# Kernel optimization log

Measured on AMD Instinct MI355X. Metric: run time of the kernel, lower is better.

## Reference

```python
import jax, jax.numpy as jnp
import numpy as np
import math

IN_DIM = 1024
OUT_DIM = 1024
GRID_SIZE = 5
SPLINE_ORDER = 3
N_COEFFS = GRID_SIZE + SPLINE_ORDER          # 8
N_KNOTS = GRID_SIZE + 2 * SPLINE_ORDER + 1   # 12
EPS = 1e-08


def setup_inputs() -> dict:
    key = jax.random.key(0)
    k_x, k_c, k_w = jax.random.split(key, 3)
    B = 4096
    x = jax.random.normal(k_x, (B, IN_DIM), dtype=jnp.float32)
    coeffs = jax.random.normal(k_c, (OUT_DIM, IN_DIM * N_COEFFS), dtype=jnp.float32) * 0.1
    # kaiming_uniform(a=sqrt(5)) -> U(-bound, bound), bound = sqrt(6/((1+a^2)*fan_in)) = 1/sqrt(fan_in)
    bound = 1.0 / math.sqrt(IN_DIM)
    base_weight = jax.random.uniform(k_w, (OUT_DIM, IN_DIM), dtype=jnp.float32,
                                     minval=-bound, maxval=bound)
    step = 2.0 / GRID_SIZE
    init_val = math.log(math.exp(step) - 1.0)
    grid_steps_log = jnp.full((IN_DIM, N_KNOTS - 1), init_val, dtype=jnp.float32)
    grid_start = jnp.full((IN_DIM, 1), -1.0 - SPLINE_ORDER * step, dtype=jnp.float32)
    res_scale = jnp.zeros((1,), dtype=jnp.float32)
    return {"x": x, "coeffs": coeffs, "base_weight": base_weight,
            "grid_steps_log": grid_steps_log, "grid_start": grid_start,
            "res_scale": res_scale}


def _get_grid(grid_steps_log, grid_start):
    steps = jax.nn.softplus(grid_steps_log)            # [in, n_knots-1]
    grid = jnp.concatenate([grid_start, steps], axis=-1)
    return jnp.cumsum(grid, axis=-1)                   # [in, n_knots]


def _b_spline(x, grid):
    # x: [B, in], grid: [in, n_knots] -> bases: [B, in, n_coeffs]
    x_u = x[:, :, None]                                # [B, in, 1]
    g = grid[None, :, :]                               # [1, in, n_knots]
    bases = ((x_u >= g[:, :, :-1]) & (x_u < g[:, :, 1:])).astype(x.dtype)
    for d in range(1, SPLINE_ORDER + 1):
        left = (x_u - g[:, :, :-(d + 1)]) / (g[:, :, d:-1] - g[:, :, :-(d + 1)] + EPS)
        right = (g[:, :, d + 1:] - x_u) / (g[:, :, d + 1:] - g[:, :, 1:-d] + EPS)
        bases = left * bases[:, :, :-1] + right * bases[:, :, 1:]
    return bases


def reference(x, coeffs, base_weight, grid_steps_log, grid_start, res_scale):
    grid = _get_grid(grid_steps_log, grid_start)
    spline_basis = _b_spline(x, grid)                  # [B, in, n_coeffs]
    B = spline_basis.shape[0]
    spline_flat = spline_basis.reshape(B, -1)          # [B, in*n_coeffs]
    spline_out = spline_flat @ coeffs.T                # [B, out]
    base_out = jax.nn.silu(x) @ base_weight.T          # [B, out]
    y = spline_out + base_out
    y = y + res_scale * x                              # residual (in_dim == out_dim)
    return y
```

## Files before the change

kernel.cpp:

```cpp
#include <hip/hip_runtime.h>

#define IN_DIM   1024
#define OUT_DIM  1024
#define BATCH    4096
#define NC       8
#define NK       12
#define KSPLINE  (IN_DIM * NC)
#define KDIM     (KSPLINE + IN_DIM)
#define EPS      1e-8f

#define NBLK_A   ((IN_DIM / 256) * (BATCH / 16))
#define NBLK_W   ((OUT_DIM * (KDIM / 4)) / 256)

#define BM       128
#define BN       64
#define BKQ      32
#define NKT      (KDIM / BKQ)
#define NGBLK    ((BATCH / BM) * (OUT_DIM / BN))

#define SWZ(r)   (((r) >> 1) & 3)

typedef _Float16 f16x8  __attribute__((ext_vector_type(8)));
typedef float    f32x4  __attribute__((ext_vector_type(4)));

static __device__ __forceinline__ unsigned short f2h_bits(float f) {
  _Float16 h = (_Float16)f;
  return __builtin_bit_cast(unsigned short, h);
}

static __device__ __forceinline__ void gl_lds16(const unsigned short* g, unsigned short* l) {
  __builtin_amdgcn_global_load_lds(
      (const __attribute__((address_space(1))) unsigned int*)g,
      (__attribute__((address_space(3))) unsigned int*)l, 16, 0, 0);
}

__global__ __launch_bounds__(256) void prep_k(const float* __restrict__ x,
                                              const float* __restrict__ coeffs,
                                              const float* __restrict__ bw,
                                              const float* __restrict__ gsl,
                                              const float* __restrict__ gstart,
                                              const float* __restrict__ rsp,
                                              unsigned short* __restrict__ A,
                                              unsigned short* __restrict__ W,
                                              float* __restrict__ out) {
  const int blk = blockIdx.x;
  if (blk < NBLK_A) {
    const int i  = (blk & 3) * 256 + threadIdx.x;
    const int b0 = (blk >> 2) * 16;
    const float rs = rsp[0];
    float g[NK];
    float acc = gstart[i];
    g[0] = acc;
#pragma unroll
    for (int t = 0; t < NK - 1; ++t) {
      float v  = gsl[i * (NK - 1) + t];
      float sp = (v > 20.f) ? v : log1pf(expf(v));
      acc += sp;
      g[t + 1] = acc;
    }
    float r[30];
#pragma unroll
    for (int j = 0; j < 11; ++j) r[j]      = 1.f / (g[j + 1] - g[j] + EPS);
#pragma unroll
    for (int j = 0; j < 10; ++j) r[11 + j] = 1.f / (g[j + 2] - g[j] + EPS);
#pragma unroll
    for (int j = 0; j <  9; ++j) r[21 + j] = 1.f / (g[j + 3] - g[j] + EPS);

    for (int bb = 0; bb < 16; ++bb) {
      const int b = b0 + bb;
      float xv = x[(size_t)b * IN_DIM + i];
      float bas[NK - 1];
#pragma unroll
      for (int k = 0; k < NK - 1; ++k)
        bas[k] = (xv >= g[k] && xv < g[k + 1]) ? 1.f : 0.f;
      const int off[3] = {0, 11, 21};
#pragma unroll
      for (int d = 1; d <= 3; ++d) {
#pragma unroll
        for (int k = 0; k < NK - 1 - d; ++k) {
          float left  = (xv - g[k])         * r[off[d - 1] + k];
          float right = (g[k + d + 1] - xv) * r[off[d - 1] + k + 1];
          bas[k] = left * bas[k] + right * bas[k + 1];
        }
      }
      uint4 pack;
      pack.x = (unsigned)f2h_bits(bas[0]) | ((unsigned)f2h_bits(bas[1]) << 16);
      pack.y = (unsigned)f2h_bits(bas[2]) | ((unsigned)f2h_bits(bas[3]) << 16);
      pack.z = (unsigned)f2h_bits(bas[4]) | ((unsigned)f2h_bits(bas[5]) << 16);
      pack.w = (unsigned)f2h_bits(bas[6]) | ((unsigned)f2h_bits(bas[7]) << 16);
      *(uint4*)&A[(size_t)b * KDIM + i * NC] = pack;
      float s = xv / (1.f + expf(-xv));
      A[(size_t)b * KDIM + KSPLINE + i] = f2h_bits(s);
      out[(size_t)b * OUT_DIM + i] = rs * xv;
    }
  } else {
    int idx = (blk - NBLK_A) * 256 + threadIdx.x;
    int n  = idx / (KDIM / 4);
    int k4 = (idx - n * (KDIM / 4)) * 4;
    float4 v;
    if (k4 < KSPLINE) v = *(const float4*)&coeffs[(size_t)n * KSPLINE + k4];
    else              v = *(const float4*)&bw[(size_t)n * IN_DIM + (k4 - KSPLINE)];
    ushort4 o;
    o.x = f2h_bits(v.x); o.y = f2h_bits(v.y); o.z = f2h_bits(v.z); o.w = f2h_bits(v.w);
    *(ushort4*)&W[(size_t)n * KDIM + k4] = o;
  }
}

__global__ __launch_bounds__(256, 2) void gemm_k(const unsigned short* __restrict__ A,
                                                 const unsigned short* __restrict__ W,
                                                 float* __restrict__ out) {
  __shared__ __align__(16) unsigned short As[4][BM][BKQ];
  __shared__ __align__(16) unsigned short Bs[4][BN][BKQ];
  const int tid  = threadIdx.x;
  const int wave = tid >> 6;
  const int lane = tid & 63;

  const int xcd = blockIdx.x & 7;
  const int idx = blockIdx.x >> 3;
  const int bm  = xcd * 4 + (idx & 3);
  const int bn  = idx >> 2;

  const int srow = wave * 16 + (lane >> 2);
  const int scsw = ((lane & 3) ^ SWZ(srow)) * 8;
  const unsigned short* aG = A + (size_t)(bm * BM + srow) * KDIM + scsw;
  const unsigned short* bG = W + (size_t)(bn * BN + srow) * KDIM + scsw;

#define STAGE(t) do {                                                          \
    const int sl_ = (t) & 3; const int kb_ = (t) * BKQ;                        \
    gl_lds16(aG + kb_,                     &As[sl_][wave * 16][0]);            \
    gl_lds16(aG + (size_t)64 * KDIM + kb_, &As[sl_][64 + wave * 16][0]);       \
    gl_lds16(bG + kb_,                     &Bs[sl_][wave * 16][0]);            \
  } while (0)

  const int l15 = lane & 15;
  const int kg  = lane >> 4;
  const int wm  = (wave >> 1) * 64;
  const int wn  = (wave & 1) * 32;

  f32x4 acc[4][2] = {};

  STAGE(0); STAGE(1); STAGE(2);
  asm volatile("s_waitcnt vmcnt(6)" ::: "memory");
  __builtin_amdgcn_s_barrier();

#pragma unroll 4
  for (int kt = 0; kt < NKT; ++kt) {
    const unsigned short* as = &As[kt & 3][0][0];
    const unsigned short* bs = &Bs[kt & 3][0][0];
    f16x8 af[4], bf[2];
#pragma unroll
    for (int mt = 0; mt < 4; ++mt) {
      int row = wm + mt * 16 + l15;
      af[mt] = *(const f16x8*)&as[row * BKQ + ((kg ^ SWZ(row)) * 8)];
    }
#pragma unroll
    for (int nt = 0; nt < 2; ++nt) {
      int row = wn + nt * 16 + l15;
      bf[nt] = *(const f16x8*)&bs[row * BKQ + ((kg ^ SWZ(row)) * 8)];
    }
    if (kt < NKT - 3) STAGE(kt + 3);
    __builtin_amdgcn_sched_barrier(0);
    __builtin_amdgcn_s_setprio(1);
#pragma unroll
    for (int mt = 0; mt < 4; ++mt)
#pragma unroll
      for (int nt = 0; nt < 2; ++nt)
        acc[mt][nt] = __builtin_amdgcn_mfma_f32_16x16x32_f16(af[mt], bf[nt], acc[mt][nt], 0, 0, 0);
    __builtin_amdgcn_s_setprio(0);
    if (kt < NKT - 3)       asm volatile("s_waitcnt vmcnt(6)" ::: "memory");
    else if (kt == NKT - 3) asm volatile("s_waitcnt vmcnt(3)" ::: "memory");
    else if (kt == NKT - 2) asm volatile("s_waitcnt vmcnt(0)" ::: "memory");
    if (kt < NKT - 1) __builtin_amdgcn_s_barrier();
  }
#undef STAGE

#pragma unroll
  for (int mt = 0; mt < 4; ++mt) {
#pragma unroll
    for (int reg = 0; reg < 4; ++reg) {
      const int row = bm * BM + wm + mt * 16 + kg * 4 + reg;
      float* orow = out + (size_t)row * OUT_DIM;
#pragma unroll
      for (int nt = 0; nt < 2; ++nt) {
        const int col = bn * BN + wn + nt * 16 + l15;
        orow[col] += acc[mt][nt][reg];
      }
    }
  }
}

extern "C" void kernel_launch(void* const* d_in, const int* in_sizes, int n_in,
                              void* d_out, int out_size, void* d_ws, size_t ws_size,
                              hipStream_t stream) {
  const float* x      = (const float*)d_in[0];
  const float* coeffs = (const float*)d_in[1];
  const float* bw     = (const float*)d_in[2];
  const float* gsl    = (const float*)d_in[3];
  const float* gstart = (const float*)d_in[4];
  const float* rsp    = (const float*)d_in[5];

  char* ws = (char*)d_ws;
  unsigned short* A  = (unsigned short*)ws;
  unsigned short* W  = (unsigned short*)(ws + (size_t)BATCH * KDIM * 2);
  float*          out = (float*)d_out;

  prep_k<<<NBLK_A + NBLK_W, 256, 0, stream>>>(x, coeffs, bw, gsl, gstart, rsp, A, W, out);
  gemm_k<<<NGBLK, 256, 0, stream>>>(A, W, out);
}
```

Baseline: 247.5 us.

## Enlarge GEMM tiles to 256x128 with 512 threads and split-K by two

The GEMM block tile grows from 128x64 to 256x128 with 512 threads, so each wave computes a 64x64 sub-tile, which raises data reuse per LDS load. To keep enough blocks for the CUs, K is split in two. The second half writes partials to a workspace buffer that a new reduce kernel adds into the output, or falls back to atomics if the workspace is too small. This adds an extra launch and about 32MB of extra traffic, drops the sched_barrier, and uses more registers and LDS, which may lower occupancy.

New measurement: 241.4 us. 1.03x faster.

```diff
diff --git a/kernel.cpp b/kernel.cpp
--- a/kernel.cpp
+++ b/kernel.cpp
@@ -12,11 +12,13 @@
 #define NBLK_A   ((IN_DIM / 256) * (BATCH / 16))
 #define NBLK_W   ((OUT_DIM * (KDIM / 4)) / 256)
 
-#define BM       128
-#define BN       64
+#define BM       256
+#define BN       128
 #define BKQ      32
-#define NKT      (KDIM / BKQ)
-#define NGBLK    ((BATCH / BM) * (OUT_DIM / BN))
+#define KSPLIT   2
+#define KPS      (KDIM / KSPLIT)
+#define NKT      (KPS / BKQ)
+#define NGBLK    ((BATCH / BM) * (OUT_DIM / BN) * KSPLIT)
 
 #define SWZ(r)   (((r) >> 1) & 3)
 
@@ -66,6 +68,7 @@
 #pragma unroll
     for (int j = 0; j <  9; ++j) r[21 + j] = 1.f / (g[j + 3] - g[j] + EPS);
 
+#pragma unroll 4
     for (int bb = 0; bb < 16; ++bb) {
       const int b = b0 + bb;
       float xv = x[(size_t)b * IN_DIM + i];
@@ -106,38 +109,40 @@
   }
 }
 
-__global__ __launch_bounds__(256, 2) void gemm_k(const unsigned short* __restrict__ A,
+__global__ __launch_bounds__(512, 2) void gemm_k(const unsigned short* __restrict__ A,
                                                  const unsigned short* __restrict__ W,
-                                                 float* __restrict__ out) {
+                                                 float* __restrict__ out,
+                                                 float* __restrict__ P,
+                                                 int use_partial) {
   __shared__ __align__(16) unsigned short As[4][BM][BKQ];
   __shared__ __align__(16) unsigned short Bs[4][BN][BKQ];
   const int tid  = threadIdx.x;
   const int wave = tid >> 6;
   const int lane = tid & 63;
 
-  const int xcd = blockIdx.x & 7;
-  const int idx = blockIdx.x >> 3;
-  const int bm  = xcd * 4 + (idx & 3);
-  const int bn  = idx >> 2;
-
-  const int srow = wave * 16 + (lane >> 2);
-  const int scsw = ((lane & 3) ^ SWZ(srow)) * 8;
-  const unsigned short* aG = A + (size_t)(bm * BM + srow) * KDIM + scsw;
-  const unsigned short* bG = W + (size_t)(bn * BN + srow) * KDIM + scsw;
+  const int s  = (blockIdx.x & 7) * 32 + (blockIdx.x >> 3);
+  const int ks = s >> 7;
+  const int bn = (s >> 4) & 7;
+  const int bm = s & 15;
+
+  const int srow = tid >> 2;
+  const int scsw = ((tid & 3) ^ SWZ(srow)) * 8;
+  const unsigned short* aG = A + (size_t)(bm * BM + srow) * KDIM + (size_t)ks * KPS + scsw;
+  const unsigned short* bG = W + (size_t)(bn * BN + srow) * KDIM + (size_t)ks * KPS + scsw;
 
 #define STAGE(t) do {                                                          \
     const int sl_ = (t) & 3; const int kb_ = (t) * BKQ;                        \
-    gl_lds16(aG + kb_,                     &As[sl_][wave * 16][0]);            \
-    gl_lds16(aG + (size_t)64 * KDIM + kb_, &As[sl_][64 + wave * 16][0]);       \
-    gl_lds16(bG + kb_,                     &Bs[sl_][wave * 16][0]);            \
+    gl_lds16(aG + kb_,                      &As[sl_][wave * 16][0]);           \
+    gl_lds16(aG + (size_t)128 * KDIM + kb_, &As[sl_][128 + wave * 16][0]);     \
+    gl_lds16(bG + kb_,                      &Bs[sl_][wave * 16][0]);           \
   } while (0)
 
   const int l15 = lane & 15;
   const int kg  = lane >> 4;
   const int wm  = (wave >> 1) * 64;
-  const int wn  = (wave & 1) * 32;
-
-  f32x4 acc[4][2] = {};
+  const int wn  = (wave & 1) * 64;
+
+  f32x4 acc[4][4] = {};
 
   STAGE(0); STAGE(1); STAGE(2);
   asm volatile("s_waitcnt vmcnt(6)" ::: "memory");
@@ -147,24 +152,23 @@
   for (int kt = 0; kt < NKT; ++kt) {
     const unsigned short* as = &As[kt & 3][0][0];
     const unsigned short* bs = &Bs[kt & 3][0][0];
-    f16x8 af[4], bf[2];
+    f16x8 af[4], bf[4];
 #pragma unroll
     for (int mt = 0; mt < 4; ++mt) {
       int row = wm + mt * 16 + l15;
       af[mt] = *(const f16x8*)&as[row * BKQ + ((kg ^ SWZ(row)) * 8)];
     }
 #pragma unroll
-    for (int nt = 0; nt < 2; ++nt) {
+    for (int nt = 0; nt < 4; ++nt) {
       int row = wn + nt * 16 + l15;
       bf[nt] = *(const f16x8*)&bs[row * BKQ + ((kg ^ SWZ(row)) * 8)];
     }
     if (kt < NKT - 3) STAGE(kt + 3);
-    __builtin_amdgcn_sched_barrier(0);
     __builtin_amdgcn_s_setprio(1);
 #pragma unroll
     for (int mt = 0; mt < 4; ++mt)
 #pragma unroll
-      for (int nt = 0; nt < 2; ++nt)
+      for (int nt = 0; nt < 4; ++nt)
         acc[mt][nt] = __builtin_amdgcn_mfma_f32_16x16x32_f16(af[mt], bf[nt], acc[mt][nt], 0, 0, 0);
     __builtin_amdgcn_s_setprio(0);
     if (kt < NKT - 3)       asm volatile("s_waitcnt vmcnt(6)" ::: "memory");
@@ -179,13 +183,30 @@
 #pragma unroll
     for (int reg = 0; reg < 4; ++reg) {
       const int row = bm * BM + wm + mt * 16 + kg * 4 + reg;
-      float* orow = out + (size_t)row * OUT_DIM;
-#pragma unroll
-      for (int nt = 0; nt < 2; ++nt) {
+      const size_t ro = (size_t)row * OUT_DIM;
+#pragma unroll
+      for (int nt = 0; nt < 4; ++nt) {
         const int col = bn * BN + wn + nt * 16 + l15;
-        orow[col] += acc[mt][nt][reg];
+        const float v = acc[mt][nt][reg];
+        if (use_partial) {
+          if (ks == 0) out[ro + col] += v;
+          else         P[ro + col]    = v;
+        } else {
+          atomicAdd(&out[ro + col], v);
+        }
       }
     }
+  }
+}
+
+__global__ __launch_bounds__(256) void reduce_k(float* __restrict__ out,
+                                                const float* __restrict__ P) {
+  const int n4 = (BATCH * OUT_DIM) / 4;
+  for (int i = blockIdx.x * 256 + threadIdx.x; i < n4; i += gridDim.x * 256) {
+    float4 o = ((const float4*)out)[i];
+    float4 p = ((const float4*)P)[i];
+    o.x += p.x; o.y += p.y; o.z += p.z; o.w += p.w;
+    ((float4*)out)[i] = o;
   }
 }
 
@@ -199,11 +220,17 @@
   const float* gstart = (const float*)d_in[4];
   const float* rsp    = (const float*)d_in[5];
 
+  const size_t szA = (size_t)BATCH * KDIM * 2;
+  const size_t szW = (size_t)OUT_DIM * KDIM * 2;
+  const size_t szP = (size_t)BATCH * OUT_DIM * 4;
   char* ws = (char*)d_ws;
   unsigned short* A  = (unsigned short*)ws;
-  unsigned short* W  = (unsigned short*)(ws + (size_t)BATCH * KDIM * 2);
+  unsigned short* W  = (unsigned short*)(ws + szA);
+  float*          P  = (float*)(ws + szA + szW);
   float*          out = (float*)d_out;
+  const int use_partial = (ws_size >= szA + szW + szP) ? 1 : 0;
 
   prep_k<<<NBLK_A + NBLK_W, 256, 0, stream>>>(x, coeffs, bw, gsl, gstart, rsp, A, W, out);
-  gemm_k<<<NGBLK, 256, 0, stream>>>(A, W, out);
-}
+  gemm_k<<<NGBLK, 512, 0, stream>>>(A, W, out, P, use_partial);
+  if (use_partial) reduce_k<<<2048, 256, 0, stream>>>(out, P);
+}
```
